# Kernel optimization log

Hardware: AMD Instinct MI355X
Metric: run time of the kernel (lower is better)

## Reference

```python
import jax, jax.numpy as jnp
import numpy as np

NV, NE = 2048, 8192
IN_V, OUT_V, IN_E = 128, 128, 128


def setup_inputs() -> dict:
    key = jax.random.key(0)
    ks = jax.random.split(key, 8)
    stdv = 1.0 / np.sqrt(OUT_V)
    return {
        "H_v": jax.random.normal(ks[0], (NV, IN_V), jnp.float32),
        "H_e": jax.random.normal(ks[1], (NE, IN_E), jnp.float32),
        "adj_e": jax.random.uniform(ks[2], (NE, NE), jnp.float32),
        "adj_v": jax.random.uniform(ks[3], (NV, NV), jnp.float32),
        "T": jax.random.uniform(ks[4], (NV, NE), jnp.float32),
        "weight": jax.random.uniform(ks[5], (IN_V, OUT_V), jnp.float32, -stdv, stdv),
        "p": jax.random.normal(ks[6], (1, IN_E), jnp.float32),
        "bias": jax.random.uniform(ks[7], (OUT_V,), jnp.float32, -stdv, stdv),
    }


def reference(H_v, H_e, adj_e, adj_v, T, weight, p, bias):
    # node_layer=True branch.
    # edge scalar weights: diag(H_e @ p^T) -> just a vector of length NE
    w = (H_e @ p.T)[:, 0]                      # [NE]
    # T @ diag(w) @ T^T == (T * w) @ T^T  (column-scale then GEMM)
    multiplier1 = (T * w[None, :]) @ T.T       # [NV, NV]
    eye = jnp.eye(multiplier1.shape[0], dtype=multiplier1.dtype)
    M1 = eye + (1.0 - eye) * multiplier1       # ones on diag, multiplier1 off-diag
    adjusted_A = M1 * adj_v                    # masked adjacency
    ret = adjusted_A @ (H_v @ weight) + bias   # [NV, OUT_V]
    return (ret, H_e)
```

## Files before the change

### kernel.cpp

```cpp
#include <hip/hip_runtime.h>
#include <hip/hip_bf16.h>
#include <stdint.h>
#include <stddef.h>

#define NV 2048
#define NE 8192
#define KSPLIT 8
#define KCHUNK (NE / KSPLIT)
#define KSPLIT2 16
#define KCHUNK2 (NV / KSPLIT2)

typedef __bf16 bf16_t;
typedef __bf16 bf16x4 __attribute__((ext_vector_type(4)));
typedef __bf16 bf16x8 __attribute__((ext_vector_type(8)));
typedef float f32x4 __attribute__((ext_vector_type(4)));
typedef float f32x16 __attribute__((ext_vector_type(16)));

__device__ static inline void load_lds16(const void* g, void* lds) {
  __builtin_amdgcn_global_load_lds(
      (const __attribute__((address_space(1))) void*)g,
      (__attribute__((address_space(3))) void*)lds,
      16, 0, 0);
}

__device__ static inline void tile_decode(int tile, int& bi, int& bj) {
  int b = (int)((sqrtf(8.f * tile + 1.f) - 1.f) * 0.5f);
  while ((b + 1) * (b + 2) / 2 <= tile) b++;
  while (b * (b + 1) / 2 > tile) b--;
  bi = b;
  bj = tile - b * (b + 1) / 2;
}

__global__ void k_w(const float* __restrict__ He, const float* __restrict__ p,
                    float* __restrict__ w) {
  int wave = threadIdx.x >> 6;
  int lane = threadIdx.x & 63;
  int e = blockIdx.x * 4 + wave;
  float v = He[(size_t)e * 128 + lane] * p[lane]
          + He[(size_t)e * 128 + 64 + lane] * p[64 + lane];
#pragma unroll
  for (int off = 32; off > 0; off >>= 1) v += __shfl_down(v, off, 64);
  if (lane == 0) w[e] = v;
}

__global__ void k_conv(const float* __restrict__ T, const float* __restrict__ w,
                       bf16_t* __restrict__ A, bf16_t* __restrict__ B) {
  size_t idx = (size_t)blockIdx.x * 256 + threadIdx.x;
  size_t base = idx * 4;
  int col = (int)(base & (NE - 1));
  f32x4 t = *(const f32x4*)(T + base);
  f32x4 w4 = *(const f32x4*)(w + col);
  bf16x4 a, b;
  a.x = (bf16_t)(t.x * w4.x); a.y = (bf16_t)(t.y * w4.y);
  a.z = (bf16_t)(t.z * w4.z); a.w = (bf16_t)(t.w * w4.w);
  b.x = (bf16_t)t.x; b.y = (bf16_t)t.y; b.z = (bf16_t)t.z; b.w = (bf16_t)t.w;
  *(bf16x4*)(A + base) = a;
  *(bf16x4*)(B + base) = b;
}

__global__ void k_hw(const float* __restrict__ Hv, const float* __restrict__ Wt,
                     bf16_t* __restrict__ HWt) {
  int t = blockIdx.x * 256 + threadIdx.x;
  int o = t & 127, j = t >> 7;
  const float* hv = Hv + (size_t)j * 128;
  float acc = 0.f;
#pragma unroll 4
  for (int k = 0; k < 128; ++k) acc += hv[k] * Wt[k * 128 + o];
  HWt[(size_t)o * NV + j] = (bf16_t)acc;
}

__global__ void __launch_bounds__(256, 4)
k_gemm1(const bf16_t* __restrict__ A, const bf16_t* __restrict__ B,
        bf16_t* __restrict__ P) {
  __shared__ bf16_t As[128 * 64];
  __shared__ bf16_t Bs[128 * 64];
  const int t = threadIdx.x;
  const int lane = t & 63;
  const int wv = t >> 6;
  const int wm = wv >> 1, wn = wv & 1;

  int bi, bj;
  tile_decode(blockIdx.x, bi, bj);
  const int i0 = bi * 128, j0 = bj * 128;
  const int kbeg = blockIdx.y * KCHUNK;
  bf16_t* Mp = P + ((size_t)blockIdx.x * KSPLIT + blockIdx.y) * 16384;

  f32x16 acc[2][2] = {};

  const int lrow = t >> 3;
  const int cb = ((t & 7) + lrow) & 7;
  const bf16_t* Ag = A + (size_t)(i0 + lrow) * NE + cb * 8;
  const bf16_t* Bg = B + (size_t)(j0 + lrow) * NE + cb * 8;

  for (int k0 = kbeg; k0 < kbeg + KCHUNK; k0 += 64) {
    __syncthreads();
#pragma unroll
    for (int it = 0; it < 4; ++it) {
      load_lds16(Ag + (size_t)(it * 32) * NE + k0, (char*)As + (it * 256 + t) * 16);
      load_lds16(Bg + (size_t)(it * 32) * NE + k0, (char*)Bs + (it * 256 + t) * 16);
    }
    __syncthreads();
#pragma unroll
    for (int kk = 0; kk < 64; kk += 16) {
      bf16x8 af[2], bfr[2];
#pragma unroll
      for (int mt = 0; mt < 2; ++mt) {
        int row = wm * 64 + mt * 32 + (lane & 31);
        int sw = (((kk >> 3) + (lane >> 5)) - row) & 7;
        af[mt] = *(const bf16x8*)&As[row * 64 + sw * 8];
      }
#pragma unroll
      for (int nt = 0; nt < 2; ++nt) {
        int row = wn * 64 + nt * 32 + (lane & 31);
        int sw = (((kk >> 3) + (lane >> 5)) - row) & 7;
        bfr[nt] = *(const bf16x8*)&Bs[row * 64 + sw * 8];
      }
#pragma unroll
      for (int mt = 0; mt < 2; ++mt)
#pragma unroll
        for (int nt = 0; nt < 2; ++nt)
          acc[mt][nt] = __builtin_amdgcn_mfma_f32_32x32x16_bf16(af[mt], bfr[nt], acc[mt][nt], 0, 0, 0);
    }
  }

#pragma unroll
  for (int mt = 0; mt < 2; ++mt) {
#pragma unroll
    for (int nt = 0; nt < 2; ++nt) {
      int tc = wn * 64 + nt * 32 + (lane & 31);
#pragma unroll
      for (int reg = 0; reg < 16; ++reg) {
        int tr = wm * 64 + mt * 32 + (reg & 3) + 8 * (reg >> 2) + 4 * (lane >> 5);
        Mp[tr * 128 + tc] = (bf16_t)acc[mt][nt][reg];
      }
    }
  }
}

__global__ void k_mask(const bf16_t* __restrict__ P, const float* __restrict__ adj_v,
                       bf16_t* __restrict__ adjA) {
  __shared__ float Ms[128 * 129];
  const int t = threadIdx.x;
  int bi, bj;
  tile_decode(blockIdx.x, bi, bj);
  const int i0 = bi * 128, j0 = bj * 128;
  const bool diag = (bi == bj);
  const bf16_t* Pt = P + (size_t)blockIdx.x * (KSPLIT * 16384);
#pragma unroll 2
  for (int c = 0; c < 8; ++c) {
    int e0 = (c * 256 + t) * 8;
    int r = e0 >> 7, col = e0 & 127;
    float v[8] = {};
#pragma unroll
    for (int s = 0; s < KSPLIT; ++s) {
      bf16x8 pv = *(const bf16x8*)(Pt + s * 16384 + e0);
#pragma unroll
      for (int u = 0; u < 8; ++u) v[u] += (float)pv[u];
    }
    size_t g = (size_t)(i0 + r) * NV + j0 + col;
    f32x4 av0 = *(const f32x4*)(adj_v + g);
    f32x4 av1 = *(const f32x4*)(adj_v + g + 4);
    bf16x8 outv;
#pragma unroll
    for (int u = 0; u < 8; ++u) {
      float vv = (diag && r == col + u) ? 1.0f : v[u];
      outv[u] = (bf16_t)(vv * (u < 4 ? av0[u] : av1[u - 4]));
    }
    *(bf16x8*)(adjA + g) = outv;
    if (!diag) {
#pragma unroll
      for (int u = 0; u < 8; ++u) Ms[(col + u) * 129 + r] = v[u];
    }
  }
  if (diag) return;
  __syncthreads();
#pragma unroll 2
  for (int c = 0; c < 8; ++c) {
    int e0 = (c * 256 + t) * 8;
    int r = e0 >> 7, col = e0 & 127;
    size_t g = (size_t)(j0 + r) * NV + i0 + col;
    f32x4 av0 = *(const f32x4*)(adj_v + g);
    f32x4 av1 = *(const f32x4*)(adj_v + g + 4);
    bf16x8 outv;
#pragma unroll
    for (int u = 0; u < 8; ++u)
      outv[u] = (bf16_t)(Ms[r * 129 + col + u] * (u < 4 ? av0[u] : av1[u - 4]));
    *(bf16x8*)(adjA + g) = outv;
  }
}

__global__ void k_gemm2(const bf16_t* __restrict__ adjA, const bf16_t* __restrict__ HWt,
                        float* __restrict__ P2) {
  __shared__ bf16_t As[128 * 64];
  __shared__ bf16_t Bs[128 * 64];
  const int t = threadIdx.x;
  const int lane = t & 63;
  const int wv = t >> 6;
  const int wm = wv >> 1, wn = wv & 1;
  const int i0 = blockIdx.x * 128;
  const int kbeg = blockIdx.y * KCHUNK2;
  float* Pp = P2 + (size_t)blockIdx.y * (NV * 128);

  f32x4 acc[4][4] = {};

  const int lrow = t >> 3;
  const int cb = ((t & 7) + lrow) & 7;
  const bf16_t* Ag = adjA + (size_t)(i0 + lrow) * NV + cb * 8;
  const bf16_t* Bg = HWt + (size_t)lrow * NV + cb * 8;

  for (int k0 = kbeg; k0 < kbeg + KCHUNK2; k0 += 64) {
    __syncthreads();
#pragma unroll
    for (int it = 0; it < 4; ++it) {
      load_lds16(Ag + (size_t)(it * 32) * NV + k0, (char*)As + (it * 256 + t) * 16);
      load_lds16(Bg + (size_t)(it * 32) * NV + k0, (char*)Bs + (it * 256 + t) * 16);
    }
    __syncthreads();
#pragma unroll
    for (int kk = 0; kk < 64; kk += 32) {
      bf16x8 af[4], bfr[4];
#pragma unroll
      for (int mt = 0; mt < 4; ++mt) {
        int row = wm * 64 + mt * 16 + (lane & 15);
        int sw = (((kk >> 3) + (lane >> 4)) - row) & 7;
        af[mt] = *(const bf16x8*)&As[row * 64 + sw * 8];
      }
#pragma unroll
      for (int nt = 0; nt < 4; ++nt) {
        int row = wn * 64 + nt * 16 + (lane & 15);
        int sw = (((kk >> 3) + (lane >> 4)) - row) & 7;
        bfr[nt] = *(const bf16x8*)&Bs[row * 64 + sw * 8];
      }
#pragma unroll
      for (int mt = 0; mt < 4; ++mt)
#pragma unroll
        for (int nt = 0; nt < 4; ++nt)
          acc[mt][nt] = __builtin_amdgcn_mfma_f32_16x16x32_bf16(af[mt], bfr[nt], acc[mt][nt], 0, 0, 0);
    }
  }

#pragma unroll
  for (int mt = 0; mt < 4; ++mt) {
#pragma unroll
    for (int nt = 0; nt < 4; ++nt) {
      int gc = wn * 64 + nt * 16 + (lane & 15);
#pragma unroll
      for (int r = 0; r < 4; ++r) {
        int gr = i0 + wm * 64 + mt * 16 + (lane >> 4) * 4 + r;
        Pp[(size_t)gr * 128 + gc] = acc[mt][nt][r];
      }
    }
  }
}

__global__ void k_bias(const float* __restrict__ P2, const float* __restrict__ bias,
                       const float* __restrict__ He, float* __restrict__ out) {
  int b = blockIdx.x;
  if (b < 256) {
    int idx = (b * 256 + threadIdx.x) * 4;
    f32x4 acc = {};
#pragma unroll
    for (int s = 0; s < KSPLIT2; ++s)
      acc += *(const f32x4*)(P2 + (size_t)s * NV * 128 + idx);
    f32x4 bb = *(const f32x4*)(bias + (idx & 127));
    *(f32x4*)(out + idx) = acc + bb;
  } else {
    size_t idx = ((size_t)(b - 256) * 256 + threadIdx.x) * 4;
    *(f32x4*)(out + (size_t)NV * 128 + idx) = *(const f32x4*)(He + idx);
  }
}

extern "C" void kernel_launch(void* const* d_in, const int* in_sizes, int n_in,
                              void* d_out, int out_size, void* d_ws, size_t ws_size,
                              hipStream_t stream) {
  const float* Hv     = (const float*)d_in[0];
  const float* He     = (const float*)d_in[1];
  const float* adj_v  = (const float*)d_in[3];
  const float* T      = (const float*)d_in[4];
  const float* weight = (const float*)d_in[5];
  const float* p      = (const float*)d_in[6];
  const float* bias   = (const float*)d_in[7];
  float* out = (float*)d_out;

  char* ws = (char*)d_ws;
  bf16_t* A_bf  = (bf16_t*)ws;
  bf16_t* B_bf  = (bf16_t*)(ws + 33554432);
  bf16_t* P1    = (bf16_t*)(ws + 67108864);
  bf16_t* adjAb = (bf16_t*)(ws + 104857600);
  float*  P2    = (float*)(ws + 113246208);
  bf16_t* HWt   = (bf16_t*)(ws + 130023424);
  float*  w     = (float*)(ws + 130547712);

  k_w<<<NE / 4, 256, 0, stream>>>(He, p, w);
  k_conv<<<(NV * NE / 4) / 256, 256, 0, stream>>>(T, w, A_bf, B_bf);
  k_hw<<<(NV * 128) / 256, 256, 0, stream>>>(Hv, weight, HWt);
  dim3 g1(136, KSPLIT);
  k_gemm1<<<g1, 256, 0, stream>>>(A_bf, B_bf, P1);
  k_mask<<<136, 256, 0, stream>>>(P1, adj_v, adjAb);
  dim3 g2(NV / 128, KSPLIT2);
  k_gemm2<<<g2, 256, 0, stream>>>(adjAb, HWt, P2);
  k_bias<<<256 + (NE * 128) / (4 * 256), 256, 0, stream>>>(P2, bias, He, out);
}
```

Measured before the change: 478.8 us.

## Enlarge gemm1 tiles to 256x256 with 512 threads and 7-way K split

The symmetric T·diag(w)·Tᵀ GEMM now uses 256x256 output tiles over 36 triangular block pairs, computed by 512-thread workgroups with 8 waves, each holding a 128x64 accumulator. The K split drops from 8 to 7 chunks of 1152, with the last chunk taking the remainder. The mask kernel is remapped to read 128x128 quadrants out of the larger partial tiles. The aim is to raise arithmetic intensity per LDS load and cut partial-sum traffic (36x7 partials instead of 136x8). The cost is more accumulator registers per wave, a larger LDS footprint, and extra redundant work on the diagonal tiles.

```diff
diff --git a/kernel.cpp b/kernel.cpp
--- a/kernel.cpp
+++ b/kernel.cpp
@@ -5,8 +5,7 @@
 
 #define NV 2048
 #define NE 8192
-#define KSPLIT 8
-#define KCHUNK (NE / KSPLIT)
+#define NSPLIT1 7
 #define KSPLIT2 16
 #define KCHUNK2 (NV / KSPLIT2)
 
@@ -69,43 +68,45 @@
   HWt[(size_t)o * NV + j] = (bf16_t)acc;
 }
 
-__global__ void __launch_bounds__(256, 4)
+__global__ void __launch_bounds__(512, 2)
 k_gemm1(const bf16_t* __restrict__ A, const bf16_t* __restrict__ B,
         bf16_t* __restrict__ P) {
-  __shared__ bf16_t As[128 * 64];
-  __shared__ bf16_t Bs[128 * 64];
+  __shared__ bf16_t As[256 * 64];
+  __shared__ bf16_t Bs[256 * 64];
   const int t = threadIdx.x;
   const int lane = t & 63;
   const int wv = t >> 6;
-  const int wm = wv >> 1, wn = wv & 1;
-
-  int bi, bj;
-  tile_decode(blockIdx.x, bi, bj);
-  const int i0 = bi * 128, j0 = bj * 128;
-  const int kbeg = blockIdx.y * KCHUNK;
-  bf16_t* Mp = P + ((size_t)blockIdx.x * KSPLIT + blockIdx.y) * 16384;
-
-  f32x16 acc[2][2] = {};
+  const int wm = wv >> 2, wn = wv & 3;
+
+  int Bi, Bj;
+  tile_decode(blockIdx.x, Bi, Bj);
+  const int i0 = Bi * 256, j0 = Bj * 256;
+  const int y = blockIdx.y;
+  const int kbeg = y * 1152;
+  const int kend = (y == 6) ? NE : kbeg + 1152;
+  bf16_t* Mp = P + ((size_t)blockIdx.x * NSPLIT1 + y) * 65536;
+
+  f32x16 acc[4][2] = {};
 
   const int lrow = t >> 3;
   const int cb = ((t & 7) + lrow) & 7;
   const bf16_t* Ag = A + (size_t)(i0 + lrow) * NE + cb * 8;
   const bf16_t* Bg = B + (size_t)(j0 + lrow) * NE + cb * 8;
 
-  for (int k0 = kbeg; k0 < kbeg + KCHUNK; k0 += 64) {
+  for (int k0 = kbeg; k0 < kend; k0 += 64) {
     __syncthreads();
 #pragma unroll
     for (int it = 0; it < 4; ++it) {
-      load_lds16(Ag + (size_t)(it * 32) * NE + k0, (char*)As + (it * 256 + t) * 16);
-      load_lds16(Bg + (size_t)(it * 32) * NE + k0, (char*)Bs + (it * 256 + t) * 16);
+      load_lds16(Ag + (size_t)(it * 64) * NE + k0, (char*)As + it * 8192 + t * 16);
+      load_lds16(Bg + (size_t)(it * 64) * NE + k0, (char*)Bs + it * 8192 + t * 16);
     }
     __syncthreads();
 #pragma unroll
     for (int kk = 0; kk < 64; kk += 16) {
-      bf16x8 af[2], bfr[2];
-#pragma unroll
-      for (int mt = 0; mt < 2; ++mt) {
-        int row = wm * 64 + mt * 32 + (lane & 31);
+      bf16x8 af[4], bfr[2];
+#pragma unroll
+      for (int mt = 0; mt < 4; ++mt) {
+        int row = wm * 128 + mt * 32 + (lane & 31);
         int sw = (((kk >> 3) + (lane >> 5)) - row) & 7;
         af[mt] = *(const bf16x8*)&As[row * 64 + sw * 8];
       }
@@ -116,7 +117,7 @@
         bfr[nt] = *(const bf16x8*)&Bs[row * 64 + sw * 8];
       }
 #pragma unroll
-      for (int mt = 0; mt < 2; ++mt)
+      for (int mt = 0; mt < 4; ++mt)
 #pragma unroll
         for (int nt = 0; nt < 2; ++nt)
           acc[mt][nt] = __builtin_amdgcn_mfma_f32_32x32x16_bf16(af[mt], bfr[nt], acc[mt][nt], 0, 0, 0);
@@ -124,14 +125,14 @@
   }
 
 #pragma unroll
-  for (int mt = 0; mt < 2; ++mt) {
+  for (int mt = 0; mt < 4; ++mt) {
 #pragma unroll
     for (int nt = 0; nt < 2; ++nt) {
       int tc = wn * 64 + nt * 32 + (lane & 31);
 #pragma unroll
       for (int reg = 0; reg < 16; ++reg) {
-        int tr = wm * 64 + mt * 32 + (reg & 3) + 8 * (reg >> 2) + 4 * (lane >> 5);
-        Mp[tr * 128 + tc] = (bf16_t)acc[mt][nt][reg];
+        int tr = wm * 128 + mt * 32 + (reg & 3) + 8 * (reg >> 2) + 4 * (lane >> 5);
+        Mp[tr * 256 + tc] = (bf16_t)acc[mt][nt][reg];
       }
     }
   }
@@ -145,15 +146,19 @@
   tile_decode(blockIdx.x, bi, bj);
   const int i0 = bi * 128, j0 = bj * 128;
   const bool diag = (bi == bj);
-  const bf16_t* Pt = P + (size_t)blockIdx.x * (KSPLIT * 16384);
+  const int Bi = bi >> 1, Bj = bj >> 1;
+  const int qa = bi & 1, qb = bj & 1;
+  const int st = Bi * (Bi + 1) / 2 + Bj;
+  const bf16_t* Pt = P + (size_t)st * (NSPLIT1 * 65536)
+                   + (size_t)(qa * 128) * 256 + qb * 128;
 #pragma unroll 2
   for (int c = 0; c < 8; ++c) {
     int e0 = (c * 256 + t) * 8;
     int r = e0 >> 7, col = e0 & 127;
     float v[8] = {};
 #pragma unroll
-    for (int s = 0; s < KSPLIT; ++s) {
-      bf16x8 pv = *(const bf16x8*)(Pt + s * 16384 + e0);
+    for (int s = 0; s < NSPLIT1; ++s) {
+      bf16x8 pv = *(const bf16x8*)(Pt + (size_t)s * 65536 + r * 256 + col);
 #pragma unroll
       for (int u = 0; u < 8; ++u) v[u] += (float)pv[u];
     }
@@ -294,8 +299,8 @@
   k_w<<<NE / 4, 256, 0, stream>>>(He, p, w);
   k_conv<<<(NV * NE / 4) / 256, 256, 0, stream>>>(T, w, A_bf, B_bf);
   k_hw<<<(NV * 128) / 256, 256, 0, stream>>>(Hv, weight, HWt);
-  dim3 g1(136, KSPLIT);
-  k_gemm1<<<g1, 256, 0, stream>>>(A_bf, B_bf, P1);
+  dim3 g1(36, NSPLIT1);
+  k_gemm1<<<g1, 512, 0, stream>>>(A_bf, B_bf, P1);
   k_mask<<<136, 256, 0, stream>>>(P1, adj_v, adjAb);
   dim3 g2(NV / 128, KSPLIT2);
   k_gemm2<<<g2, 256, 0, stream>>>(adjAb, HWt, P2);
```

Result: faster. 456.3 us (-4.7%).
